# Kernel tuning notes

Measured on AMD Instinct MI355X. Metric: run time of the kernel, lower is better.

Reference implementation:

```python
import jax, jax.numpy as jnp
import numpy as np

NUM_BRANCHES = 4
REP_DIM = 1024
FEAT_DIM = 128
N_DATA = 100000
NCE_K = 4096
NCE_T = 0.07
BATCH = 128
EPS = 1e-07


def setup_inputs() -> dict:
    key = jax.random.key(0)
    ks = jax.random.split(key, 8)
    d = {}
    for i in range(NUM_BRANCHES):
        d[f"emb{i}"] = jax.random.normal(ks[i], (BATCH, REP_DIM), dtype=jnp.float32)
    d["W"] = jax.random.normal(ks[4], (NUM_BRANCHES, FEAT_DIM, REP_DIM), dtype=jnp.float32) * 0.03
    d["b"] = jnp.zeros((NUM_BRANCHES, FEAT_DIM), dtype=jnp.float32)
    stdv = 1.0 / np.sqrt(FEAT_DIM / 3.0)
    d["memory"] = jax.random.uniform(ks[5], (NUM_BRANCHES, N_DATA, FEAT_DIM), dtype=jnp.float32, minval=-stdv, maxval=stdv)
    idx = jax.random.randint(ks[6], (BATCH,), 0, N_DATA)
    neg = jax.random.randint(ks[7], (BATCH, NCE_K), 0, N_DATA)
    d["idx"] = idx
    d["contrast_idx"] = jnp.concatenate([idx[:, None], neg], axis=1)  # col 0 = positive
    return d


def reference(emb0, emb1, emb2, emb3, W, b, memory, idx, contrast_idx):
    # per-branch Embed: flatten -> Linear -> L2 normalize
    embs = jnp.stack([emb0, emb1, emb2, emb3], axis=0)            # [R,B,rep]
    h = jnp.einsum('rbi,rdi->rbd', embs, W) + b[:, None, :]        # [R,B,D]
    e = h / jnp.sqrt(jnp.sum(h * h, axis=-1, keepdims=True))       # Normalize(power=2)

    # ContrastMemory: gather K+1 bank rows per sample per branch (detached)
    w = jax.lax.stop_gradient(memory[:, contrast_idx, :])          # [R,B,K+1,D]
    # scores[i,j,b,k] = <bank_j row, emb_i>  for every ordered pair
    scores = jnp.einsum('jbkd,ibd->ijbk', w, e)                    # [R,R,B,K+1]
    out = jnp.exp(scores / NCE_T)
    Z = jax.lax.stop_gradient(jnp.mean(out, axis=(2, 3)) * N_DATA)  # per-pair Z estimate
    out = out / Z[:, :, None, None]

    # ContrastLoss (Eq 11)
    m = float(NCE_K)
    Pn = 1.0 / float(N_DATA)
    pos = out[:, :, :, 0]                                          # [R,R,B]
    neg = out[:, :, :, 1:]                                         # [R,R,B,K]
    log_D1 = jnp.log(pos / (pos + m * Pn + EPS))
    log_D0 = jnp.log((m * Pn) / (neg + m * Pn + EPS))
    per_pair = -(jnp.sum(log_D1, axis=2) + jnp.sum(log_D0, axis=(2, 3))) / BATCH
    mask = 1.0 - jnp.eye(NUM_BRANCHES, dtype=per_pair.dtype)       # only i != j pairs
    return jnp.sum(per_pair * mask)
```

## Files before the change

### kernel.cpp

```cpp
#include <hip/hip_runtime.h>
#include <math.h>

#define NBR    4
#define REP    1024
#define FD     128
#define NDATA  100000
#define KP1    4097
#define BN     128
#define MPN    0.04096f
#define EPS_C  1e-7f
#define TINV   (1.0f / 0.07f)
#define NSLOT  64
#define TREFS  (BN * KP1)
#define NWAVE  8192

typedef unsigned int   uint4e   __attribute__((ext_vector_type(4)));
typedef unsigned short ushort4e __attribute__((ext_vector_type(4)));
typedef _Float16       half2e   __attribute__((ext_vector_type(2)));
typedef float          floatx4  __attribute__((ext_vector_type(4)));

static __device__ __forceinline__ unsigned short f2h(float f) {
    union { _Float16 h; unsigned short u; } c; c.h = (_Float16)f; return c.u;
}
static __device__ __forceinline__ float h_lo(unsigned int u) {
    union { unsigned int u; _Float16 h[2]; } c; c.u = u; return (float)c.h[0];
}
static __device__ __forceinline__ float h_hi(unsigned int u) {
    union { unsigned int u; _Float16 h[2]; } c; c.u = u; return (float)c.h[1];
}
static __device__ __forceinline__ half2e u2h2(unsigned int u) {
    union { unsigned int u; half2e h; } c; c.u = u; return c.h;
}
static __device__ __forceinline__ unsigned short f2bf(float f) {
    union { float f; unsigned int u; } c; c.f = f;
    unsigned int u = c.u;
    u += 0x7fffu + ((u >> 16) & 1u);
    return (unsigned short)(u >> 16);
}
static __device__ __forceinline__ float bf2f(unsigned short h) {
    union { unsigned int u; float f; } c; c.u = ((unsigned int)h) << 16;
    return c.f;
}

__global__ void k_feat(const float* __restrict__ e0, const float* __restrict__ e1,
                       const float* __restrict__ e2, const float* __restrict__ e3,
                       const float* __restrict__ W, const float* __restrict__ bias,
                       float* __restrict__ e_out, ushort* __restrict__ eh16) {
    const int r = blockIdx.x;
    const int b = blockIdx.y;
    const float* emb = (r == 0 ? e0 : r == 1 ? e1 : r == 2 ? e2 : e3) + (size_t)b * REP;

    __shared__ float s_emb[REP];
    for (int i = threadIdx.x; i < REP; i += blockDim.x) s_emb[i] = emb[i];
    __syncthreads();

    const int d = threadIdx.x;
    const float4* wrow = (const float4*)(W + ((size_t)r * FD + d) * REP);
    float acc = 0.f;
#pragma unroll 8
    for (int c = 0; c < REP / 4; ++c) {
        float4 v = wrow[c];
        acc += v.x * s_emb[4*c+0] + v.y * s_emb[4*c+1]
             + v.z * s_emb[4*c+2] + v.w * s_emb[4*c+3];
    }
    float h = acc + bias[r * FD + d];

    __shared__ float red[FD];
    red[d] = h * h;
    __syncthreads();
    for (int off = FD / 2; off > 0; off >>= 1) {
        if (d < off) red[d] += red[d + off];
        __syncthreads();
    }
    float nrm = sqrtf(red[0]);
    float val = h / nrm;
    e_out[((size_t)r * BN + b) * FD + d] = val;
    if (eh16) eh16[((size_t)r * BN + b) * FD + d] = f2h(val);
}

__global__ void k_hist(const int* __restrict__ cidx, int* __restrict__ counts) {
    const int k = blockIdx.x * 256 + threadIdx.x;
    if (k >= KP1) return;
    const int b = blockIdx.y;
    atomicAdd(&counts[cidx[(size_t)b * KP1 + k]], 1);
}

__global__ void k_assign(const int* __restrict__ counts, int* __restrict__ start,
                         int* __restrict__ cursor) {
    __shared__ int s[256];
    __shared__ int sbase;
    const int tid = threadIdx.x;
    const int n = blockIdx.x * 256 + tid;
    int c = (n < NDATA) ? counts[n] : 0;
    s[tid] = c;
    __syncthreads();
#pragma unroll
    for (int off = 1; off < 256; off <<= 1) {
        int v = (tid >= off) ? s[tid - off] : 0;
        __syncthreads();
        s[tid] += v;
        __syncthreads();
    }
    if (tid == 255) sbase = atomicAdd(cursor, s[255]);
    __syncthreads();
    if (n < NDATA) start[n] = sbase + s[tid] - c;
}

__global__ void k_scatter(const int* __restrict__ cidx, const int* __restrict__ start,
                          int* __restrict__ fill, unsigned long long* __restrict__ inv64) {
    const int k = blockIdx.x * 256 + threadIdx.x;
    if (k >= KP1) return;
    const int b = blockIdx.y;
    const int n = cidx[(size_t)b * KP1 + k];
    const int pos = atomicAdd(&fill[n], 1);
    inv64[(size_t)start[n] + pos] =
        ((unsigned long long)(unsigned int)n << 20) |
        ((unsigned long long)(unsigned int)b << 13) |
        (unsigned long long)(unsigned int)k;
}

__global__ __launch_bounds__(256)
void k_pass1i(const float* __restrict__ mem, const ushort* __restrict__ eh16,
              const unsigned long long* __restrict__ inv64,
              float* __restrict__ Zsl, ushort* __restrict__ expS) {
    const int lane = threadIdx.x & 63;
    const int w    = threadIdx.x >> 6;
    const int g    = (blockIdx.x << 2) + w;
    const int l4   = lane & 15;
    const int jj   = lane >> 4;
    const int d0   = l4 * 8;
    const bool b3  = (l4 & 8) != 0;
    const bool b2  = (l4 & 4) != 0;

    const int base = g * 64 + (g < 128 ? g : 128);
    const int end  = base + 64 + (g < 128 ? 1 : 0);

    const float* mrow_base = mem + (size_t)jj * NDATA * FD + d0;
    const ushort* eb_base  = eh16 + d0;

    float z = 0.f;
    int n_prev = -1;
    half2e mh[4];
    mh[0] = half2e{(_Float16)0.f, (_Float16)0.f};
    mh[1] = mh[0]; mh[2] = mh[0]; mh[3] = mh[0];

    unsigned long long vnext = inv64[base];
    for (int c = base; c < end; ++c) {
        const unsigned long long v = vnext;
        if (c + 1 < end) vnext = inv64[c + 1];
        const int n = (int)(v >> 20);
        const unsigned int bk = (unsigned int)v & 0xFFFFFu;
        const int b = (int)(bk >> 13);
        const int k = (int)(bk & 8191u);

        const ushort* eb = eb_base + (size_t)b * FD;
        uint4 ev0 = *(const uint4*)(eb);
        uint4 ev1 = *(const uint4*)(eb + (size_t)1 * BN * FD);
        uint4 ev2 = *(const uint4*)(eb + (size_t)2 * BN * FD);
        uint4 ev3 = *(const uint4*)(eb + (size_t)3 * BN * FD);

        if (n != n_prev) {
            const floatx4* mp = (const floatx4*)(mrow_base + (size_t)n * FD);
            floatx4 v0 = __builtin_nontemporal_load(mp);
            floatx4 v1 = __builtin_nontemporal_load(mp + 1);
            mh[0] = half2e{(_Float16)v0.x, (_Float16)v0.y};
            mh[1] = half2e{(_Float16)v0.z, (_Float16)v0.w};
            mh[2] = half2e{(_Float16)v1.x, (_Float16)v1.y};
            mh[3] = half2e{(_Float16)v1.z, (_Float16)v1.w};
            n_prev = n;
        }

        float a0 = 0.f, a1 = 0.f, a2 = 0.f, a3 = 0.f;
#pragma unroll
        for (int q = 0; q < 4; ++q) {
            half2e hw = mh[q];
            a0 = __builtin_amdgcn_fdot2(hw, u2h2((&ev0.x)[q]), a0, false);
            a1 = __builtin_amdgcn_fdot2(hw, u2h2((&ev1.x)[q]), a1, false);
            a2 = __builtin_amdgcn_fdot2(hw, u2h2((&ev2.x)[q]), a2, false);
            a3 = __builtin_amdgcn_fdot2(hw, u2h2((&ev3.x)[q]), a3, false);
        }
        float t0 = __shfl_xor(b3 ? a0 : a2, 8, 64);
        float t1 = __shfl_xor(b3 ? a1 : a3, 8, 64);
        float c0 = (b3 ? a2 : a0) + t0;
        float c1 = (b3 ? a3 : a1) + t1;
        float t2 = __shfl_xor(b2 ? c0 : c1, 4, 64);
        float d  = (b2 ? c1 : c0) + t2;
        d += __shfl_xor(d, 2, 64);
        d += __shfl_xor(d, 1, 64);
        float x = __expf(d * TINV);
        z += x;
        if ((lane & 3) == 0)
            expS[((size_t)b * KP1 + k) * 16 + (lane >> 2)] = f2h(x);
    }

    __shared__ float s_z[4][16];
    const int i = ((l4 >> 3) << 1) | ((l4 >> 2) & 1);
    if ((lane & 3) == 0) s_z[w][i * 4 + jj] = z;
    __syncthreads();
    if (threadIdx.x < 16) {
        float vv = s_z[0][threadIdx.x] + s_z[1][threadIdx.x]
                 + s_z[2][threadIdx.x] + s_z[3][threadIdx.x];
        const int slot = blockIdx.x & (NSLOT - 1);
        atomicAdd(&Zsl[slot * 16 + threadIdx.x], vv);
    }
}

__global__ void k_zred(const float* __restrict__ Zsl, float* __restrict__ Zsum) {
    if (threadIdx.x < 16) {
        float s = 0.f;
        for (int sl = 0; sl < NSLOT; ++sl) s += Zsl[sl * 16 + threadIdx.x];
        Zsum[threadIdx.x] = s;
    }
}

static __device__ __forceinline__ void acc_words(const uint4& p0, const uint4& p1,
                                                 const float* __restrict__ s_zinv,
                                                 float* __restrict__ acc, bool pos) {
    unsigned int wds[8] = {p0.x, p0.y, p0.z, p0.w, p1.x, p1.y, p1.z, p1.w};
#pragma unroll
    for (int w = 0; w < 8; ++w) {
        float v0 = h_lo(wds[w]) * s_zinv[2*w];
        float v1 = h_hi(wds[w]) * s_zinv[2*w+1];
        if (pos) {
            acc[2*w]   += -__logf(1.f + (MPN + EPS_C) / v0);
            acc[2*w+1] += -__logf(1.f + (MPN + EPS_C) / v1);
        } else {
            acc[2*w]   += -__logf(1.f + (v0 + EPS_C) * (1.f / MPN));
            acc[2*w+1] += -__logf(1.f + (v1 + EPS_C) * (1.f / MPN));
        }
    }
}

__global__ __launch_bounds__(256)
void k_pass2f(const uint4* __restrict__ expS, const float* __restrict__ Zsum,
              float* __restrict__ Asl) {
    const int b = blockIdx.y;

    __shared__ float s_zinv[16];
    if (threadIdx.x < 16) {
        int jj = threadIdx.x >> 2, ii = threadIdx.x & 3;
        float Z = Zsum[ii * 4 + jj] *
                  (float)((double)NDATA / ((double)BN * (double)KP1));
        s_zinv[threadIdx.x] = 1.0f / Z;
    }
    __syncthreads();

    const uint4* es = expS + (size_t)b * (KP1 * 2);
    const int base = threadIdx.x + blockIdx.x * 256;

    float acc[16];
#pragma unroll
    for (int t = 0; t < 16; ++t) acc[t] = 0.f;

#pragma unroll
    for (int it = 0; it < 2; ++it) {
        const int k = base + it * 2048;
        uint4 p0 = es[(size_t)k * 2];
        uint4 p1 = es[(size_t)k * 2 + 1];
        acc_words(p0, p1, s_zinv, acc, k == 0);
    }
    if (base == 0) {
        uint4 p0 = es[(size_t)4096 * 2];
        uint4 p1 = es[(size_t)4096 * 2 + 1];
        acc_words(p0, p1, s_zinv, acc, false);
    }

#pragma unroll
    for (int t = 0; t < 16; ++t) {
#pragma unroll
        for (int off = 32; off > 0; off >>= 1)
            acc[t] += __shfl_down(acc[t], off, 64);
    }
    __shared__ float s_a[4][16];
    const int w = threadIdx.x >> 6;
    if ((threadIdx.x & 63) == 0) {
#pragma unroll
        for (int t = 0; t < 16; ++t) s_a[w][t] = acc[t];
    }
    __syncthreads();
    if (threadIdx.x < 16) {
        float v = s_a[0][threadIdx.x] + s_a[1][threadIdx.x]
                + s_a[2][threadIdx.x] + s_a[3][threadIdx.x];
        const int slot = (blockIdx.y * gridDim.x + blockIdx.x) & (NSLOT - 1);
        atomicAdd(&Asl[slot * 16 + threadIdx.x], v);
    }
}

__global__ void k_final_slots(const float* __restrict__ Asl, float* __restrict__ out) {
    const int tid = threadIdx.x;
    const int comp = tid & 15;
    const int grp  = tid >> 4;
    float a = 0.f;
    for (int sl = grp; sl < NSLOT; sl += 16) a += Asl[sl * 16 + comp];
    const float m = ((comp >> 2) != (comp & 3)) ? 1.f : 0.f;
    __shared__ float s[256];
    s[tid] = a * m;
    __syncthreads();
    for (int off = 128; off > 0; off >>= 1) {
        if (tid < off) s[tid] += s[tid + off];
        __syncthreads();
    }
    if (tid == 0) out[0] = -s[0] / (float)BN;
}

static __device__ __forceinline__ void dot4(const float4* __restrict__ row,
                                            const float* __restrict__ se,
                                            float& a0, float& a1, float& a2, float& a3) {
    a0 = a1 = a2 = a3 = 0.f;
#pragma unroll 8
    for (int c = 0; c < FD / 4; ++c) {
        float4 v = row[c];
        const int o = 4 * c;
        a0 += v.x * se[0*FD+o+0] + v.y * se[0*FD+o+1] + v.z * se[0*FD+o+2] + v.w * se[0*FD+o+3];
        a1 += v.x * se[1*FD+o+0] + v.y * se[1*FD+o+1] + v.z * se[1*FD+o+2] + v.w * se[1*FD+o+3];
        a2 += v.x * se[2*FD+o+0] + v.y * se[2*FD+o+1] + v.z * se[2*FD+o+2] + v.w * se[2*FD+o+3];
        a3 += v.x * se[3*FD+o+0] + v.y * se[3*FD+o+1] + v.z * se[3*FD+o+2] + v.w * se[3*FD+o+3];
    }
}

static __device__ __forceinline__ void block_reduce4(float z0, float z1, float z2,
                                                     float z3, float* dst, int j) {
    __shared__ float sred[256];
    float zs[NBR] = {z0, z1, z2, z3};
    for (int i = 0; i < NBR; ++i) {
        sred[threadIdx.x] = zs[i];
        __syncthreads();
        for (int off = 128; off > 0; off >>= 1) {
            if ((int)threadIdx.x < off) sred[threadIdx.x] += sred[threadIdx.x + off];
            __syncthreads();
        }
        if (threadIdx.x == 0) atomicAdd(&dst[i * NBR + j], sred[0]);
        __syncthreads();
    }
}

static __device__ __forceinline__ float term_of(float ex, float zinv, int k) {
    const float c = MPN + EPS_C;
    float v = ex * zinv;
    if (k == 0) return -__logf(1.0f + c / v);
    return -__logf(1.0f + (v + EPS_C) * (1.0f / MPN));
}

template <bool STORE>
__global__ void k_pass1_f32(const float* __restrict__ e, const float* __restrict__ memory,
                            const int* __restrict__ cidx,
                            float* __restrict__ Zsum, ushort4* __restrict__ expS) {
    const int j = blockIdx.z;
    const int b = blockIdx.y;

    __shared__ float s_e[NBR * FD];
    for (int t = threadIdx.x; t < NBR * FD; t += blockDim.x) {
        int i = t >> 7, d = t & (FD - 1);
        s_e[t] = e[((size_t)i * BN + b) * FD + d];
    }
    __syncthreads();

    const int* ci = cidx + (size_t)b * KP1;
    const float4* mem4 = (const float4*)(memory + (size_t)j * NDATA * FD);
    float z0 = 0.f, z1 = 0.f, z2 = 0.f, z3 = 0.f;

    for (int k = threadIdx.x + blockIdx.x * blockDim.x; k < KP1;
         k += blockDim.x * gridDim.x) {
        const int n = ci[k];
        const float4* row = mem4 + (size_t)n * (FD / 4);
        float a0, a1, a2, a3;
        dot4(row, s_e, a0, a1, a2, a3);
        float x0 = __expf(a0 * TINV);
        float x1 = __expf(a1 * TINV);
        float x2 = __expf(a2 * TINV);
        float x3 = __expf(a3 * TINV);
        z0 += x0; z1 += x1; z2 += x2; z3 += x3;
        if (STORE) {
            ushort4 st;
            st.x = f2bf(x0); st.y = f2bf(x1); st.z = f2bf(x2); st.w = f2bf(x3);
            expS[((size_t)j * BN + b) * KP1 + k] = st;
        }
    }
    block_reduce4(z0, z1, z2, z3, Zsum, j);
}

__global__ void k_pass2_stored(const ushort4* __restrict__ expS,
                               const float* __restrict__ Zsum,
                               float* __restrict__ accum) {
    const int j = blockIdx.z;
    const int b = blockIdx.y;

    __shared__ float s_zinv[NBR];
    if (threadIdx.x < NBR) {
        float Z = Zsum[threadIdx.x * NBR + j] *
                  (float)((double)NDATA / ((double)BN * (double)KP1));
        s_zinv[threadIdx.x] = 1.0f / Z;
    }
    __syncthreads();

    const ushort4* es = expS + ((size_t)j * BN + b) * KP1;
    float a0 = 0.f, a1 = 0.f, a2 = 0.f, a3 = 0.f;

    for (int k = threadIdx.x + blockIdx.x * blockDim.x; k < KP1;
         k += blockDim.x * gridDim.x) {
        ushort4 v = es[k];
        a0 += term_of(bf2f(v.x), s_zinv[0], k);
        a1 += term_of(bf2f(v.y), s_zinv[1], k);
        a2 += term_of(bf2f(v.z), s_zinv[2], k);
        a3 += term_of(bf2f(v.w), s_zinv[3], k);
    }
    block_reduce4(a0, a1, a2, a3, accum, j);
}

__global__ void k_pass2_regather(const float* __restrict__ e, const float* __restrict__ memory,
                                 const int* __restrict__ cidx,
                                 const float* __restrict__ Zsum, float* __restrict__ accum) {
    const int j = blockIdx.z;
    const int b = blockIdx.y;

    __shared__ float s_e[NBR * FD];
    __shared__ float s_zinv[NBR];
    for (int t = threadIdx.x; t < NBR * FD; t += blockDim.x) {
        int i = t >> 7, d = t & (FD - 1);
        s_e[t] = e[((size_t)i * BN + b) * FD + d];
    }
    if (threadIdx.x < NBR) {
        float Z = Zsum[threadIdx.x * NBR + j] *
                  (float)((double)NDATA / ((double)BN * (double)KP1));
        s_zinv[threadIdx.x] = 1.0f / Z;
    }
    __syncthreads();

    const int* ci = cidx + (size_t)b * KP1;
    const float4* mem4 = (const float4*)(memory + (size_t)j * NDATA * FD);
    float a0s = 0.f, a1s = 0.f, a2s = 0.f, a3s = 0.f;

    for (int k = threadIdx.x + blockIdx.x * blockDim.x; k < KP1;
         k += blockDim.x * gridDim.x) {
        const int n = ci[k];
        const float4* row = mem4 + (size_t)n * (FD / 4);
        float a0, a1, a2, a3;
        dot4(row, s_e, a0, a1, a2, a3);
        a0s += term_of(__expf(a0 * TINV), s_zinv[0], k);
        a1s += term_of(__expf(a1 * TINV), s_zinv[1], k);
        a2s += term_of(__expf(a2 * TINV), s_zinv[2], k);
        a3s += term_of(__expf(a3 * TINV), s_zinv[3], k);
    }
    block_reduce4(a0s, a1s, a2s, a3s, accum, j);
}

__global__ void k_init(float* __restrict__ p, int n) {
    int i = blockIdx.x * blockDim.x + threadIdx.x;
    if (i < n) p[i] = 0.f;
}

__global__ void k_final_legacy(const float* __restrict__ accum, float* __restrict__ out) {
    if (threadIdx.x == 0) {
        float s = 0.f;
        for (int i = 0; i < NBR; ++i)
            for (int j = 0; j < NBR; ++j)
                if (i != j) s += -accum[i * NBR + j] / (float)BN;
        out[0] = s;
    }
}

extern "C" void kernel_launch(void* const* d_in, const int* in_sizes, int n_in,
                              void* d_out, int out_size, void* d_ws, size_t ws_size,
                              hipStream_t stream) {
    const float* e0   = (const float*)d_in[0];
    const float* e1   = (const float*)d_in[1];
    const float* e2   = (const float*)d_in[2];
    const float* e3   = (const float*)d_in[3];
    const float* W    = (const float*)d_in[4];
    const float* bias = (const float*)d_in[5];
    const float* mem  = (const float*)d_in[6];
    const int*   cidx = (const int*)d_in[8];
    float* out = (float*)d_out;

    float* ws    = (float*)d_ws;
    float* e     = ws;
    float* Zsum  = ws + 65536;
    float* accum = ws + 65552;
    float* Zsl   = ws + 65568;
    float* Asl   = ws + 66592;
    const size_t base_b   = (size_t)67616 * 4;
    const size_t eh16_b   = (size_t)NBR * BN * FD * 2;
    const size_t cnt_b    = (size_t)NDATA * 4;
    const size_t cur_b    = 16;
    const size_t inv_b    = (size_t)TREFS * 8;
    const size_t expS_b   = (size_t)BN * KP1 * 16 * 2;

    const size_t off_eh16   = base_b;
    const size_t off_counts = off_eh16 + eh16_b;
    const size_t off_fill   = off_counts + cnt_b;
    const size_t off_cursor = off_fill + cnt_b;
    const size_t off_start  = off_cursor + cur_b;
    const size_t off_inv    = off_start + cnt_b;
    const size_t off_expS   = off_inv + inv_b;

    const size_t need_full = off_expS + expS_b;
    const size_t need_mid  = base_b + expS_b;

    if (ws_size >= need_full) {
        ushort* eh16 = (ushort*)((char*)d_ws + off_eh16);
        int* counts  = (int*)((char*)d_ws + off_counts);
        int* fill    = (int*)((char*)d_ws + off_fill);
        int* cursor  = (int*)((char*)d_ws + off_cursor);
        int* start   = (int*)((char*)d_ws + off_start);
        unsigned long long* inv64 = (unsigned long long*)((char*)d_ws + off_inv);
        ushort* expS = (ushort*)((char*)d_ws + off_expS);

        k_init<<<9, 256, 0, stream>>>(Zsum, 2080);
        k_init<<<782, 256, 0, stream>>>((float*)counts, 200004);
        k_feat<<<dim3(NBR, BN), 128, 0, stream>>>(e0, e1, e2, e3, W, bias, e, eh16);
        k_hist<<<dim3(17, BN), 256, 0, stream>>>(cidx, counts);
        k_assign<<<391, 256, 0, stream>>>(counts, start, cursor);
        k_scatter<<<dim3(17, BN), 256, 0, stream>>>(cidx, start, fill, inv64);
        k_pass1i<<<2048, 256, 0, stream>>>(mem, eh16, inv64, Zsl, expS);
        k_zred<<<1, 64, 0, stream>>>(Zsl, Zsum);
        k_pass2f<<<dim3(8, BN), 256, 0, stream>>>((const uint4*)expS, Zsum, Asl);
        k_final_slots<<<1, 256, 0, stream>>>(Asl, out);
    } else if (ws_size >= need_mid) {
        k_init<<<9, 256, 0, stream>>>(Zsum, 2080);
        k_feat<<<dim3(NBR, BN), 128, 0, stream>>>(e0, e1, e2, e3, W, bias, e, nullptr);
        ushort4* expS = (ushort4*)((char*)d_ws + base_b);
        k_pass1_f32<true><<<dim3(4, BN, NBR), 256, 0, stream>>>(e, mem, cidx, Zsum, expS);
        k_pass2_stored<<<dim3(4, BN, NBR), 256, 0, stream>>>(expS, Zsum, accum);
        k_final_legacy<<<1, 64, 0, stream>>>(accum, out);
    } else {
        k_init<<<9, 256, 0, stream>>>(Zsum, 2080);
        k_feat<<<dim3(NBR, BN), 128, 0, stream>>>(e0, e1, e2, e3, W, bias, e, nullptr);
        k_pass1_f32<false><<<dim3(4, BN, NBR), 256, 0, stream>>>(e, mem, cidx, Zsum, nullptr);
        k_pass2_regather<<<dim3(4, BN, NBR), 256, 0, stream>>>(e, mem, cidx, Zsum, accum);
        k_final_legacy<<<1, 64, 0, stream>>>(accum, out);
    }
}
```

Baseline: 484.2 us.

## Fuse whole pipeline into one cooperative persistent kernel with grid syncs

```diff
diff --git a/kernel.cpp b/kernel.cpp
--- a/kernel.cpp
+++ b/kernel.cpp
@@ -1,5 +1,8 @@
 #include <hip/hip_runtime.h>
+#include <hip/hip_cooperative_groups.h>
 #include <math.h>
+
+namespace cg = cooperative_groups;
 
 #define NBR    4
 #define REP    1024
@@ -12,7 +15,6 @@
 #define TINV   (1.0f / 0.07f)
 #define NSLOT  64
 #define TREFS  (BN * KP1)
-#define NWAVE  8192
 
 typedef unsigned int   uint4e   __attribute__((ext_vector_type(4)));
 typedef unsigned short ushort4e __attribute__((ext_vector_type(4)));
@@ -40,6 +42,301 @@
 static __device__ __forceinline__ float bf2f(unsigned short h) {
     union { unsigned int u; float f; } c; c.u = ((unsigned int)h) << 16;
     return c.f;
+}
+
+static __device__ __forceinline__ void acc_words(const uint4& p0, const uint4& p1,
+                                                 const float* __restrict__ s_zinv,
+                                                 float* __restrict__ acc, bool pos) {
+    unsigned int wds[8] = {p0.x, p0.y, p0.z, p0.w, p1.x, p1.y, p1.z, p1.w};
+#pragma unroll
+    for (int w = 0; w < 8; ++w) {
+        float v0 = h_lo(wds[w]) * s_zinv[2*w];
+        float v1 = h_hi(wds[w]) * s_zinv[2*w+1];
+        if (pos) {
+            acc[2*w]   += -__logf(1.f + (MPN + EPS_C) / v0);
+            acc[2*w+1] += -__logf(1.f + (MPN + EPS_C) / v1);
+        } else {
+            acc[2*w]   += -__logf(1.f + (v0 + EPS_C) * (1.f / MPN));
+            acc[2*w+1] += -__logf(1.f + (v1 + EPS_C) * (1.f / MPN));
+        }
+    }
+}
+
+__global__ __launch_bounds__(256, 4)
+void k_all(const float* __restrict__ e0, const float* __restrict__ e1,
+           const float* __restrict__ e2, const float* __restrict__ e3,
+           const float* __restrict__ W, const float* __restrict__ bias,
+           const float* __restrict__ mem, const int* __restrict__ cidx,
+           ushort* __restrict__ eh2, int* __restrict__ counts,
+           int* __restrict__ start, int* __restrict__ fill,
+           int* __restrict__ cursor, unsigned long long* __restrict__ inv64,
+           ushort* __restrict__ expS, float* __restrict__ Zsl,
+           float* __restrict__ out) {
+    cg::grid_group grid = cg::this_grid();
+    const int tid = threadIdx.x;
+
+    __shared__ float s_emb[REP];
+    __shared__ float s_part[256];
+    __shared__ float s_sq[FD];
+    __shared__ int   s_scan[256];
+    __shared__ int   s_base;
+    __shared__ float s_z[4][16];
+    __shared__ float s_zinv[16];
+    __shared__ float s_a[4][16];
+
+    {
+        const int NT = gridDim.x * 256;
+        for (int t = blockIdx.x * 256 + tid; t < NDATA; t += NT) {
+            counts[t] = 0; fill[t] = 0;
+        }
+        for (int t = blockIdx.x * 256 + tid; t < NSLOT * 16; t += NT) Zsl[t] = 0.f;
+        if (blockIdx.x == 0 && tid == 0) { cursor[0] = 0; out[0] = 0.f; }
+    }
+    grid.sync();
+
+    {
+        const int F = (gridDim.x + 1) >> 1;
+        if ((int)blockIdx.x < F) {
+            for (int u = blockIdx.x; u < NBR * BN; u += F) {
+                const int r = u >> 7;
+                const int b = u & 127;
+                const float* emb = (r == 0 ? e0 : r == 1 ? e1 : r == 2 ? e2 : e3)
+                                   + (size_t)b * REP;
+                for (int t = tid; t < REP; t += 256) s_emb[t] = emb[t];
+                __syncthreads();
+                const int d  = tid & 127;
+                const int kh = tid >> 7;
+                const float4* wrow = (const float4*)(W + ((size_t)r * FD + d) * REP)
+                                     + kh * 128;
+                const float* se = s_emb + (kh << 9);
+                float a = 0.f;
+#pragma unroll 4
+                for (int c = 0; c < 128; ++c) {
+                    float4 v = wrow[c];
+                    a += v.x * se[4*c+0] + v.y * se[4*c+1]
+                       + v.z * se[4*c+2] + v.w * se[4*c+3];
+                }
+                s_part[tid] = a;
+                __syncthreads();
+                float h = 0.f;
+                if (kh == 0) {
+                    h = s_part[d] + s_part[128 + d] + bias[r * FD + d];
+                    s_sq[d] = h * h;
+                }
+                __syncthreads();
+                for (int off = 64; off > 0; off >>= 1) {
+                    if (tid < off) s_sq[tid] += s_sq[tid + off];
+                    __syncthreads();
+                }
+                float nrm = sqrtf(s_sq[0]);
+                if (kh == 0) {
+                    eh2[((size_t)(b * 16 + (d >> 3)) * 4 + r) * 8 + (d & 7)]
+                        = f2h(h / nrm);
+                }
+                __syncthreads();
+            }
+        } else {
+            const int NT = (gridDim.x - F) * 256;
+            for (int t = ((int)blockIdx.x - F) * 256 + tid; t < TREFS; t += NT)
+                atomicAdd(&counts[cidx[t]], 1);
+        }
+    }
+    grid.sync();
+
+    {
+        const int NCH = (NDATA + 255) / 256;
+        for (int ch = blockIdx.x; ch < NCH; ch += gridDim.x) {
+            const int n = ch * 256 + tid;
+            int c = (n < NDATA) ? counts[n] : 0;
+            s_scan[tid] = c;
+            __syncthreads();
+#pragma unroll
+            for (int off = 1; off < 256; off <<= 1) {
+                int v = (tid >= off) ? s_scan[tid - off] : 0;
+                __syncthreads();
+                s_scan[tid] += v;
+                __syncthreads();
+            }
+            if (tid == 255) s_base = atomicAdd(cursor, s_scan[255]);
+            __syncthreads();
+            if (n < NDATA) start[n] = s_base + s_scan[tid] - c;
+            __syncthreads();
+        }
+    }
+    grid.sync();
+
+    {
+        const int NT = gridDim.x * 256;
+        for (int t = blockIdx.x * 256 + tid; t < TREFS; t += NT) {
+            const int n = cidx[t];
+            const int b = t / KP1;
+            const int k = t - b * KP1;
+            const int pos = atomicAdd(&fill[n], 1);
+            inv64[(size_t)start[n] + pos] =
+                ((unsigned long long)(unsigned int)n << 20) |
+                ((unsigned long long)(unsigned int)b << 13) |
+                (unsigned long long)(unsigned int)k;
+        }
+    }
+    grid.sync();
+
+    {
+        const int lane = tid & 63;
+        const int wv   = tid >> 6;
+        const int g    = ((int)blockIdx.x << 2) + wv;
+        const int NW   = (int)gridDim.x << 2;
+        const int PER  = TREFS / NW;
+        const int REM  = TREFS - PER * NW;
+        const int base = g * PER + (g < REM ? g : REM);
+        const int end  = base + PER + (g < REM ? 1 : 0);
+        const int l4   = lane & 15;
+        const int jj   = lane >> 4;
+        const bool f3  = (l4 & 8) != 0;
+        const bool fl2 = (l4 & 4) != 0;
+
+        const float* mrow_base = mem + (size_t)jj * (NDATA * FD) + l4 * 8;
+        const uint4* e4 = (const uint4*)eh2;
+
+        float z = 0.f;
+        int n_prev = -1;
+        half2e mh0 = half2e{(_Float16)0.f, (_Float16)0.f};
+        half2e mh1 = mh0, mh2 = mh0, mh3 = mh0;
+
+        auto proc = [&](unsigned long long v, const uint4& q0, const uint4& q1,
+                        const uint4& q2, const uint4& q3) {
+            const int n = (int)(v >> 20);
+            const unsigned int bk = (unsigned int)v & 0xFFFFFu;
+            const int b = (int)(bk >> 13);
+            const int k = (int)(bk & 8191u);
+            if (n != n_prev) {
+                const floatx4* mp = (const floatx4*)(mrow_base + (size_t)n * FD);
+                floatx4 r0 = __builtin_nontemporal_load(mp);
+                floatx4 r1 = __builtin_nontemporal_load(mp + 1);
+                mh0 = half2e{(_Float16)r0.x, (_Float16)r0.y};
+                mh1 = half2e{(_Float16)r0.z, (_Float16)r0.w};
+                mh2 = half2e{(_Float16)r1.x, (_Float16)r1.y};
+                mh3 = half2e{(_Float16)r1.z, (_Float16)r1.w};
+                n_prev = n;
+            }
+            float a0 = 0.f, a1 = 0.f, a2 = 0.f, a3 = 0.f;
+            a0 = __builtin_amdgcn_fdot2(mh0, u2h2(q0.x), a0, false);
+            a0 = __builtin_amdgcn_fdot2(mh1, u2h2(q0.y), a0, false);
+            a0 = __builtin_amdgcn_fdot2(mh2, u2h2(q0.z), a0, false);
+            a0 = __builtin_amdgcn_fdot2(mh3, u2h2(q0.w), a0, false);
+            a1 = __builtin_amdgcn_fdot2(mh0, u2h2(q1.x), a1, false);
+            a1 = __builtin_amdgcn_fdot2(mh1, u2h2(q1.y), a1, false);
+            a1 = __builtin_amdgcn_fdot2(mh2, u2h2(q1.z), a1, false);
+            a1 = __builtin_amdgcn_fdot2(mh3, u2h2(q1.w), a1, false);
+            a2 = __builtin_amdgcn_fdot2(mh0, u2h2(q2.x), a2, false);
+            a2 = __builtin_amdgcn_fdot2(mh1, u2h2(q2.y), a2, false);
+            a2 = __builtin_amdgcn_fdot2(mh2, u2h2(q2.z), a2, false);
+            a2 = __builtin_amdgcn_fdot2(mh3, u2h2(q2.w), a2, false);
+            a3 = __builtin_amdgcn_fdot2(mh0, u2h2(q3.x), a3, false);
+            a3 = __builtin_amdgcn_fdot2(mh1, u2h2(q3.y), a3, false);
+            a3 = __builtin_amdgcn_fdot2(mh2, u2h2(q3.z), a3, false);
+            a3 = __builtin_amdgcn_fdot2(mh3, u2h2(q3.w), a3, false);
+            float t0 = __shfl_xor(f3 ? a0 : a2, 8, 64);
+            float t1 = __shfl_xor(f3 ? a1 : a3, 8, 64);
+            float c0 = (f3 ? a2 : a0) + t0;
+            float c1 = (f3 ? a3 : a1) + t1;
+            float t2 = __shfl_xor(fl2 ? c0 : c1, 4, 64);
+            float dd = (fl2 ? c1 : c0) + t2;
+            dd += __shfl_xor(dd, 2, 64);
+            dd += __shfl_xor(dd, 1, 64);
+            float x = __expf(dd * TINV);
+            z += x;
+            if ((lane & 3) == 0)
+                expS[((size_t)b * KP1 + k) * 16 + (lane >> 2)] = f2h(x);
+        };
+
+        uint4 qA0, qA1, qA2, qA3, qB0, qB1, qB2, qB3;
+        unsigned long long v0 = inv64[base];
+        unsigned long long v1 = (base + 1 < end) ? inv64[base + 1] : v0;
+        {
+            const uint4* p = e4 + ((size_t)(((unsigned)v0 & 0xFFFFFu) >> 13) * 16 + l4) * 4;
+            qA0 = p[0]; qA1 = p[1]; qA2 = p[2]; qA3 = p[3];
+        }
+        {
+            const uint4* p = e4 + ((size_t)(((unsigned)v1 & 0xFFFFFu) >> 13) * 16 + l4) * 4;
+            qB0 = p[0]; qB1 = p[1]; qB2 = p[2]; qB3 = p[3];
+        }
+
+        int c = base;
+        for (; c + 1 < end; c += 2) {
+            unsigned long long v2 = (c + 2 < end) ? inv64[c + 2] : v1;
+            unsigned long long v3 = (c + 3 < end) ? inv64[c + 3] : v2;
+            proc(v0, qA0, qA1, qA2, qA3);
+            {
+                const uint4* p = e4 + ((size_t)(((unsigned)v2 & 0xFFFFFu) >> 13) * 16 + l4) * 4;
+                qA0 = p[0]; qA1 = p[1]; qA2 = p[2]; qA3 = p[3];
+            }
+            proc(v1, qB0, qB1, qB2, qB3);
+            {
+                const uint4* p = e4 + ((size_t)(((unsigned)v3 & 0xFFFFFu) >> 13) * 16 + l4) * 4;
+                qB0 = p[0]; qB1 = p[1]; qB2 = p[2]; qB3 = p[3];
+            }
+            v0 = v2; v1 = v3;
+        }
+        if (c < end) proc(v0, qA0, qA1, qA2, qA3);
+
+        const int i = ((l4 >> 3) << 1) | ((l4 >> 2) & 1);
+        if ((lane & 3) == 0) s_z[wv][i * 4 + jj] = z;
+        __syncthreads();
+        if (tid < 16) {
+            float vv = s_z[0][tid] + s_z[1][tid] + s_z[2][tid] + s_z[3][tid];
+            const int slot = blockIdx.x & (NSLOT - 1);
+            atomicAdd(&Zsl[slot * 16 + tid], vv);
+        }
+    }
+    grid.sync();
+
+    {
+        if (tid < 16) {
+            const int comp = ((tid & 3) << 2) | (tid >> 2);
+            float s = 0.f;
+            for (int sl = 0; sl < NSLOT; ++sl) s += Zsl[sl * 16 + comp];
+            float Z = s * (float)((double)NDATA / ((double)BN * (double)KP1));
+            s_zinv[tid] = 1.0f / Z;
+        }
+        __syncthreads();
+
+        const uint4* esu = (const uint4*)expS;
+        float acc[16];
+#pragma unroll
+        for (int t = 0; t < 16; ++t) acc[t] = 0.f;
+
+        const int NT = gridDim.x * 256;
+        for (int t = blockIdx.x * 256 + tid; t < TREFS; t += NT) {
+            const int b = t / KP1;
+            const int k = t - b * KP1;
+            uint4 p0 = esu[(size_t)t * 2];
+            uint4 p1 = esu[(size_t)t * 2 + 1];
+            acc_words(p0, p1, s_zinv, acc, k == 0);
+        }
+
+#pragma unroll
+        for (int t = 0; t < 16; ++t) {
+#pragma unroll
+            for (int off = 32; off > 0; off >>= 1)
+                acc[t] += __shfl_down(acc[t], off, 64);
+        }
+        const int wv = tid >> 6;
+        if ((tid & 63) == 0) {
+#pragma unroll
+            for (int t = 0; t < 16; ++t) s_a[wv][t] = acc[t];
+        }
+        __syncthreads();
+        if (tid < 16) {
+            float v = s_a[0][tid] + s_a[1][tid] + s_a[2][tid] + s_a[3][tid];
+            const int jjj = tid >> 2, iii = tid & 3;
+            v = (iii != jjj) ? v : 0.f;
+            v += __shfl_down(v, 8, 64);
+            v += __shfl_down(v, 4, 64);
+            v += __shfl_down(v, 2, 64);
+            v += __shfl_down(v, 1, 64);
+            if (tid == 0) atomicAdd(out, -v / (float)BN);
+        }
+    }
 }
 
 __global__ void k_feat(const float* __restrict__ e0, const float* __restrict__ e1,
@@ -171,14 +468,23 @@
         }
 
         float a0 = 0.f, a1 = 0.f, a2 = 0.f, a3 = 0.f;
-#pragma unroll
-        for (int q = 0; q < 4; ++q) {
-            half2e hw = mh[q];
-            a0 = __builtin_amdgcn_fdot2(hw, u2h2((&ev0.x)[q]), a0, false);
-            a1 = __builtin_amdgcn_fdot2(hw, u2h2((&ev1.x)[q]), a1, false);
-            a2 = __builtin_amdgcn_fdot2(hw, u2h2((&ev2.x)[q]), a2, false);
-            a3 = __builtin_amdgcn_fdot2(hw, u2h2((&ev3.x)[q]), a3, false);
-        }
+        a0 = __builtin_amdgcn_fdot2(mh[0], u2h2(ev0.x), a0, false);
+        a0 = __builtin_amdgcn_fdot2(mh[1], u2h2(ev0.y), a0, false);
+        a0 = __builtin_amdgcn_fdot2(mh[2], u2h2(ev0.z), a0, false);
+        a0 = __builtin_amdgcn_fdot2(mh[3], u2h2(ev0.w), a0, false);
+        a1 = __builtin_amdgcn_fdot2(mh[0], u2h2(ev1.x), a1, false);
+        a1 = __builtin_amdgcn_fdot2(mh[1], u2h2(ev1.y), a1, false);
+        a1 = __builtin_amdgcn_fdot2(mh[2], u2h2(ev1.z), a1, false);
+        a1 = __builtin_amdgcn_fdot2(mh[3], u2h2(ev1.w), a1, false);
+        a2 = __builtin_amdgcn_fdot2(mh[0], u2h2(ev2.x), a2, false);
+        a2 = __builtin_amdgcn_fdot2(mh[1], u2h2(ev2.y), a2, false);
+        a2 = __builtin_amdgcn_fdot2(mh[2], u2h2(ev2.z), a2, false);
+        a2 = __builtin_amdgcn_fdot2(mh[3], u2h2(ev2.w), a2, false);
+        a3 = __builtin_amdgcn_fdot2(mh[0], u2h2(ev3.x), a3, false);
+        a3 = __builtin_amdgcn_fdot2(mh[1], u2h2(ev3.y), a3, false);
+        a3 = __builtin_amdgcn_fdot2(mh[2], u2h2(ev3.z), a3, false);
+        a3 = __builtin_amdgcn_fdot2(mh[3], u2h2(ev3.w), a3, false);
+
         float t0 = __shfl_xor(b3 ? a0 : a2, 8, 64);
         float t1 = __shfl_xor(b3 ? a1 : a3, 8, 64);
         float c0 = (b3 ? a2 : a0) + t0;
@@ -194,8 +500,9 @@
     }
 
     __shared__ float s_z[4][16];
+    const int j = lane >> 4;
     const int i = ((l4 >> 3) << 1) | ((l4 >> 2) & 1);
-    if ((lane & 3) == 0) s_z[w][i * 4 + jj] = z;
+    if ((lane & 3) == 0) s_z[w][i * 4 + j] = z;
     __syncthreads();
     if (threadIdx.x < 16) {
         float vv = s_z[0][threadIdx.x] + s_z[1][threadIdx.x]
@@ -210,24 +517,6 @@
         float s = 0.f;
         for (int sl = 0; sl < NSLOT; ++sl) s += Zsl[sl * 16 + threadIdx.x];
         Zsum[threadIdx.x] = s;
-    }
-}
-
-static __device__ __forceinline__ void acc_words(const uint4& p0, const uint4& p1,
-                                                 const float* __restrict__ s_zinv,
-                                                 float* __restrict__ acc, bool pos) {
-    unsigned int wds[8] = {p0.x, p0.y, p0.z, p0.w, p1.x, p1.y, p1.z, p1.w};
-#pragma unroll
-    for (int w = 0; w < 8; ++w) {
-        float v0 = h_lo(wds[w]) * s_zinv[2*w];
-        float v1 = h_hi(wds[w]) * s_zinv[2*w+1];
-        if (pos) {
-            acc[2*w]   += -__logf(1.f + (MPN + EPS_C) / v0);
-            acc[2*w+1] += -__logf(1.f + (MPN + EPS_C) / v1);
-        } else {
-            acc[2*w]   += -__logf(1.f + (v0 + EPS_C) * (1.f / MPN));
-            acc[2*w+1] += -__logf(1.f + (v1 + EPS_C) * (1.f / MPN));
-        }
     }
 }
 
@@ -484,6 +773,7 @@
     const size_t cur_b    = 16;
     const size_t inv_b    = (size_t)TREFS * 8;
     const size_t expS_b   = (size_t)BN * KP1 * 16 * 2;
+    const size_t eh2_b    = (size_t)BN * 16 * 4 * 8 * 2;
 
     const size_t off_eh16   = base_b;
     const size_t off_counts = off_eh16 + eh16_b;
@@ -492,11 +782,54 @@
     const size_t off_start  = off_cursor + cur_b;
     const size_t off_inv    = off_start + cnt_b;
     const size_t off_expS   = off_inv + inv_b;
-
+    const size_t off_eh2    = off_expS + expS_b;
+
+    const size_t need_coop = off_eh2 + eh2_b;
     const size_t need_full = off_expS + expS_b;
     const size_t need_mid  = base_b + expS_b;
 
-    if (ws_size >= need_full) {
+    static int s_nblk = -1;
+    if (s_nblk < 0) {
+        int nb = 0;
+        hipError_t oe = hipOccupancyMaxActiveBlocksPerMultiprocessor(
+            &nb, (const void*)k_all, 256, 0);
+        int dev = 0;
+        hipGetDevice(&dev);
+        hipDeviceProp_t prop;
+        hipError_t pe = hipGetDeviceProperties(&prop, dev);
+        if (oe == hipSuccess && pe == hipSuccess && nb > 0 &&
+            prop.multiProcessorCount > 0) {
+            long long t = (long long)nb * prop.multiProcessorCount;
+            s_nblk = (int)(t > 2048 ? 2048 : t);
+        } else {
+            s_nblk = 0;
+        }
+    }
+
+    bool done = false;
+    if (ws_size >= need_coop && s_nblk >= 64) {
+        ushort* eh2  = (ushort*)((char*)d_ws + off_eh2);
+        int* counts  = (int*)((char*)d_ws + off_counts);
+        int* start   = (int*)((char*)d_ws + off_start);
+        int* fill    = (int*)((char*)d_ws + off_fill);
+        int* cursor  = (int*)((char*)d_ws + off_cursor);
+        unsigned long long* inv64 = (unsigned long long*)((char*)d_ws + off_inv);
+        ushort* expS = (ushort*)((char*)d_ws + off_expS);
+
+        void* kargs[] = {
+            (void*)&e0, (void*)&e1, (void*)&e2, (void*)&e3,
+            (void*)&W,  (void*)&bias, (void*)&mem, (void*)&cidx,
+            (void*)&eh2, (void*)&counts, (void*)&start, (void*)&fill,
+            (void*)&cursor, (void*)&inv64, (void*)&expS, (void*)&Zsl,
+            (void*)&out
+        };
+        hipError_t le = hipLaunchCooperativeKernel(
+            (const void*)k_all, dim3(s_nblk), dim3(256), kargs, 0, stream);
+        if (le == hipSuccess) done = true;
+        else s_nblk = 0;
+    }
+
+    if (!done && ws_size >= need_full) {
         ushort* eh16 = (ushort*)((char*)d_ws + off_eh16);
         int* counts  = (int*)((char*)d_ws + off_counts);
         int* fill    = (int*)((char*)d_ws + off_fill);
@@ -515,18 +848,20 @@
         k_zred<<<1, 64, 0, stream>>>(Zsl, Zsum);
         k_pass2f<<<dim3(8, BN), 256, 0, stream>>>((const uint4*)expS, Zsum, Asl);
         k_final_slots<<<1, 256, 0, stream>>>(Asl, out);
-    } else if (ws_size >= need_mid) {
+        done = true;
+    }
+
+    if (!done) {
         k_init<<<9, 256, 0, stream>>>(Zsum, 2080);
         k_feat<<<dim3(NBR, BN), 128, 0, stream>>>(e0, e1, e2, e3, W, bias, e, nullptr);
-        ushort4* expS = (ushort4*)((char*)d_ws + base_b);
-        k_pass1_f32<true><<<dim3(4, BN, NBR), 256, 0, stream>>>(e, mem, cidx, Zsum, expS);
-        k_pass2_stored<<<dim3(4, BN, NBR), 256, 0, stream>>>(expS, Zsum, accum);
+        if (ws_size >= need_mid) {
+            ushort4* expS = (ushort4*)((char*)d_ws + base_b);
+            k_pass1_f32<true><<<dim3(4, BN, NBR), 256, 0, stream>>>(e, mem, cidx, Zsum, expS);
+            k_pass2_stored<<<dim3(4, BN, NBR), 256, 0, stream>>>(expS, Zsum, accum);
+        } else {
+            k_pass1_f32<false><<<dim3(4, BN, NBR), 256, 0, stream>>>(e, mem, cidx, Zsum, nullptr);
+            k_pass2_regather<<<dim3(4, BN, NBR), 256, 0, stream>>>(e, mem, cidx, Zsum, accum);
+        }
         k_final_legacy<<<1, 64, 0, stream>>>(accum, out);
-    } else {
-        k_init<<<9, 256, 0, stream>>>(Zsum, 2080);
-        k_feat<<<dim3(NBR, BN), 128, 0, stream>>>(e0, e1, e2, e3, W, bias, e, nullptr);
-        k_pass1_f32<false><<<dim3(4, BN, NBR), 256, 0, stream>>>(e, mem, cidx, Zsum, nullptr);
-        k_pass2_regather<<<dim3(4, BN, NBR), 256, 0, stream>>>(e, mem, cidx, Zsum, accum);
-        k_final_legacy<<<1, 64, 0, stream>>>(accum, out);
-    }
-}
+    }
+}
```

After: 836.3 us. 1.73x slower.
